# Performance work log

Hardware: AMD Instinct MI355X
Metric: run time of the kernel (lower is better)

Reference implementation:

```python
import jax, jax.numpy as jnp
import numpy as np

D_MODEL, N_HEADS, D_HEAD, D_FF, N_LAYERS, VOCAB = 768, 12, 64, 3072, 4, 32000
B, S = 4, 1024
EPS = 1e-5
NEG = -1000000000.0


def layer_norm(x, gamma, beta):
    mean = jnp.mean(x, axis=-1, keepdims=True)
    var = jnp.mean((x - mean) ** 2, axis=-1, keepdims=True)
    return gamma * ((x - mean) / jnp.sqrt(var + EPS)) + beta


def gelu_lean(x):
    return x * (0.5 * (1.0 + jnp.tanh(0.7978845608 * (x + 0.044715 * x * x * x))))


def positional_encoding(seq_len, dim, dtype):
    idx = jnp.arange(dim)
    exponent = (2 * (idx // 2)).astype(dtype) / float(dim)
    pos = jnp.arange(seq_len, dtype=dtype)[:, None]
    angle = pos / jnp.power(jnp.asarray(10000.0, dtype), exponent[None, :])
    return jnp.where((idx % 2 == 0)[None, :], jnp.sin(angle), jnp.cos(angle))


def setup_inputs() -> dict:
    key = jax.random.key(0)
    ks = jax.random.split(key, 10)
    std = 0.02
    inp = {
        "tokens": jax.random.randint(ks[0], (B, S), 0, VOCAB),
        "predict_idx": 1023,
        "embedding": std * jax.random.normal(ks[1], (D_MODEL, VOCAB), jnp.float32),
        "ln1_g": jnp.ones((N_LAYERS, D_MODEL), jnp.float32),
        "ln1_b": jnp.zeros((N_LAYERS, D_MODEL), jnp.float32),
        "wq": std * jax.random.normal(ks[2], (N_LAYERS, N_HEADS, D_HEAD, D_MODEL), jnp.float32),
        "wk": std * jax.random.normal(ks[3], (N_LAYERS, N_HEADS, D_HEAD, D_MODEL), jnp.float32),
        "wv": std * jax.random.normal(ks[4], (N_LAYERS, N_HEADS, D_HEAD, D_MODEL), jnp.float32),
        "wo": std * jax.random.normal(ks[5], (N_LAYERS, D_MODEL, N_HEADS * D_HEAD), jnp.float32),
        "ln2_g": jnp.ones((N_LAYERS, D_MODEL), jnp.float32),
        "ln2_b": jnp.zeros((N_LAYERS, D_MODEL), jnp.float32),
        "fc1": std * jax.random.normal(ks[6], (N_LAYERS, D_FF, D_MODEL), jnp.float32),
        "fc2": std * jax.random.normal(ks[7], (N_LAYERS, D_MODEL, D_FF), jnp.float32),
        "lnf_g": jnp.ones((D_MODEL,), jnp.float32),
        "lnf_b": jnp.zeros((D_MODEL,), jnp.float32),
        "unembed": std * jax.random.normal(ks[8], (VOCAB, D_MODEL), jnp.float32),
    }
    return inp


def reference(tokens, predict_idx, embedding, ln1_g, ln1_b, wq, wk, wv, wo,
              ln2_g, ln2_b, fc1, fc2, lnf_g, lnf_b, unembed):
    dtype = embedding.dtype
    b, s = tokens.shape
    d_head = wq.shape[2]
    scale = 1.0 / float(np.sqrt(d_head))

    # token embedding [B,S,D] + sinusoidal positions
    x = embedding.T[tokens] + positional_encoding(s, embedding.shape[0], dtype)[None]

    # causal mask: True above the diagonal -> filled with -1e9
    causal = jnp.triu(jnp.ones((s, s), bool), k=1)

    for l in range(wq.shape[0]):
        h = layer_norm(x, ln1_g[l], ln1_b[l])
        q = jnp.einsum('bsd,hed->bhse', h, wq[l])
        k = jnp.einsum('bsd,hed->bhse', h, wk[l])
        v = jnp.einsum('bsd,hed->bhse', h, wv[l])
        scores = jnp.einsum('bhse,bhte->bhst', q, k) * scale
        scores = jnp.where(causal[None, None], NEG, scores)
        weights = jax.nn.softmax(scores, axis=-1)
        attn = jnp.einsum('bhst,bhte->bhse', weights, v)  # [B,H,S,dh]
        attn = attn.transpose(0, 2, 1, 3).reshape(b, s, -1)  # concat heads
        x = x + attn @ wo[l].T
        h2 = layer_norm(x, ln2_g[l], ln2_b[l])
        x = x + gelu_lean(h2 @ fc1[l].T) @ fc2[l].T

    selected = x[:, predict_idx, :]  # [B, D]
    normed = layer_norm(selected, lnf_g, lnf_b)
    return normed @ unembed.T  # [B, vocab]
```

## Files before the change

### kernel.cpp

```cpp
#include <hip/hip_runtime.h>
#include <hip/hip_bf16.h>

#define D_MODEL 768
#define N_HEADS 12
#define D_HEAD  64
#define D_FF    3072
#define N_LAYERS 4
#define VOCAB   32000
#define BATCH   4
#define SEQ     1024
#define NROWS   (BATCH*SEQ)
#define NEGV    -1000000000.0f
#define LN_EPS  1e-5f

typedef __attribute__((ext_vector_type(8))) short bf16x8;
typedef __attribute__((ext_vector_type(4))) float f32x4;
typedef __attribute__((ext_vector_type(8))) unsigned short u16x8;
typedef __attribute__((ext_vector_type(4))) unsigned short u16x4;

typedef __attribute__((address_space(1))) const unsigned int g_u32;
typedef __attribute__((address_space(3))) unsigned int l_u32;

__device__ __forceinline__ float bf2f(unsigned short u) {
  return __uint_as_float(((unsigned int)u) << 16);
}
__device__ __forceinline__ unsigned short f2bf(float f) {
  __hip_bfloat16 h = __float2bfloat16(f);
  return *reinterpret_cast<unsigned short*>(&h);
}

__device__ __forceinline__ float block_reduce_sum(float v, float* sbuf) {
#pragma unroll
  for (int off = 32; off > 0; off >>= 1) v += __shfl_down(v, off, 64);
  int lane = threadIdx.x & 63, wid = threadIdx.x >> 6;
  if (lane == 0) sbuf[wid] = v;
  __syncthreads();
  if (threadIdx.x == 0) sbuf[4] = sbuf[0] + sbuf[1] + sbuf[2] + sbuf[3];
  __syncthreads();
  return sbuf[4];
}

__device__ __forceinline__ float gelu_f(float x) {
  float c = x + 0.044715f * x * x * x;
  return x * (0.5f * (1.0f + tanhf(0.7978845608f * c)));
}

__global__ __launch_bounds__(256) void convert_kernel(
    const float* __restrict__ src, __hip_bfloat16* __restrict__ dst, int n)
{
  int i = (blockIdx.x * 256 + threadIdx.x) * 8;
  if (i >= n) return;
  float4 a = *(const float4*)(src + i);
  float4 b = *(const float4*)(src + i + 4);
  struct bf8 { __hip_bfloat16 h[8]; } r;
  r.h[0] = __float2bfloat16(a.x); r.h[1] = __float2bfloat16(a.y);
  r.h[2] = __float2bfloat16(a.z); r.h[3] = __float2bfloat16(a.w);
  r.h[4] = __float2bfloat16(b.x); r.h[5] = __float2bfloat16(b.y);
  r.h[6] = __float2bfloat16(b.z); r.h[7] = __float2bfloat16(b.w);
  *(bf8*)(dst + i) = r;
}

__global__ __launch_bounds__(256) void qkv_pack_kernel(
    const float* __restrict__ wq, const float* __restrict__ wk,
    const float* __restrict__ wv, __hip_bfloat16* __restrict__ dst)
{
  const int WMAT = D_MODEL * D_MODEL;
  long long i = (long long)(blockIdx.x * 256 + threadIdx.x) * 8;
  long long l = i / (3LL * WMAT);
  long long rem = i - l * 3LL * WMAT;
  int which = (int)(rem / WMAT);
  long long off = rem - (long long)which * WMAT;
  const float* src = (which == 0 ? wq : which == 1 ? wk : wv) + l * WMAT + off;
  float4 a = *(const float4*)src;
  float4 b = *(const float4*)(src + 4);
  struct bf8 { __hip_bfloat16 h[8]; } r;
  r.h[0] = __float2bfloat16(a.x); r.h[1] = __float2bfloat16(a.y);
  r.h[2] = __float2bfloat16(a.z); r.h[3] = __float2bfloat16(a.w);
  r.h[4] = __float2bfloat16(b.x); r.h[5] = __float2bfloat16(b.y);
  r.h[6] = __float2bfloat16(b.z); r.h[7] = __float2bfloat16(b.w);
  *(bf8*)(dst + i) = r;
}

__global__ __launch_bounds__(256) void transpose_emb_kernel(
    const float* __restrict__ emb, __hip_bfloat16* __restrict__ embT)
{
  __shared__ float tile[64][65];
  const int vb = blockIdx.x * 64;
  const int db = blockIdx.y * 64;
  const int tid = threadIdx.x;
  {
    int r = tid >> 4, c = (tid & 15) * 4;
#pragma unroll
    for (int p = 0; p < 4; ++p) {
      float4 v = *(const float4*)(emb + (size_t)(db + r + p * 16) * VOCAB + vb + c);
      tile[c + 0][r + p * 16] = v.x;
      tile[c + 1][r + p * 16] = v.y;
      tile[c + 2][r + p * 16] = v.z;
      tile[c + 3][r + p * 16] = v.w;
    }
  }
  __syncthreads();
  {
    int v = tid >> 2, d0 = (tid & 3) * 16;
    unsigned short* op = (unsigned short*)embT + (size_t)(vb + v) * D_MODEL + db + d0;
    u16x8 o0, o1;
#pragma unroll
    for (int j = 0; j < 8; ++j) {
      o0[j] = f2bf(tile[v][d0 + j]);
      o1[j] = f2bf(tile[v][d0 + 8 + j]);
    }
    *(u16x8*)op = o0;
    *(u16x8*)(op + 8) = o1;
  }
}

__global__ __launch_bounds__(256) void embed_kernel(
    const int* __restrict__ tokens, const __hip_bfloat16* __restrict__ embT,
    float* __restrict__ x)
{
  int bs = blockIdx.x;
  int s = bs & (SEQ - 1);
  int tok = tokens[bs];
  const unsigned short* ep = (const unsigned short*)embT + (size_t)tok * D_MODEL;
  for (int d = threadIdx.x; d < D_MODEL; d += 256) {
    float ev = bf2f(ep[d]);
    int dpair = d & ~1;
    float expo = (float)dpair * (1.0f / (float)D_MODEL);
    float ang = (float)s / powf(10000.0f, expo);
    float pe = (d & 1) ? cosf(ang) : sinf(ang);
    x[(size_t)bs * D_MODEL + d] = ev + pe;
  }
}

__global__ __launch_bounds__(256) void ln_kernel(
    const float* __restrict__ in, __hip_bfloat16* __restrict__ out,
    const float* __restrict__ g, const float* __restrict__ bb)
{
  __shared__ float sbuf[8];
  size_t row = blockIdx.x;
  const float* rp = in + row * D_MODEL;
  int t = threadIdx.x;
  float x0 = rp[t], x1 = rp[t + 256], x2 = rp[t + 512];
  float mean = block_reduce_sum(x0 + x1 + x2, sbuf) * (1.0f / (float)D_MODEL);
  float d0 = x0 - mean, d1 = x1 - mean, d2 = x2 - mean;
  float var = block_reduce_sum(d0*d0 + d1*d1 + d2*d2, sbuf) * (1.0f / (float)D_MODEL);
  float rstd = rsqrtf(var + LN_EPS);
  __hip_bfloat16* op = out + row * D_MODEL;
  op[t]       = __float2bfloat16(g[t]       * (d0 * rstd) + bb[t]);
  op[t + 256] = __float2bfloat16(g[t + 256] * (d1 * rstd) + bb[t + 256]);
  op[t + 512] = __float2bfloat16(g[t + 512] * (d2 * rstd) + bb[t + 512]);
}

__global__ __launch_bounds__(256) void final_ln_kernel(
    const float* __restrict__ x, const int* __restrict__ pidx,
    const float* __restrict__ g, const float* __restrict__ bb,
    float* __restrict__ out)
{
  __shared__ float sbuf[8];
  int p = pidx[0];
  const float* rp = x + ((size_t)blockIdx.x * SEQ + p) * D_MODEL;
  int t = threadIdx.x;
  float x0 = rp[t], x1 = rp[t + 256], x2 = rp[t + 512];
  float mean = block_reduce_sum(x0 + x1 + x2, sbuf) * (1.0f / (float)D_MODEL);
  float d0 = x0 - mean, d1 = x1 - mean, d2 = x2 - mean;
  float var = block_reduce_sum(d0*d0 + d1*d1 + d2*d2, sbuf) * (1.0f / (float)D_MODEL);
  float rstd = rsqrtf(var + LN_EPS);
  float* op = out + (size_t)blockIdx.x * D_MODEL;
  op[t]       = g[t]       * (d0 * rstd) + bb[t];
  op[t + 256] = g[t + 256] * (d1 * rstd) + bb[t + 256];
  op[t + 512] = g[t + 512] * (d2 * rstd) + bb[t + 512];
}

__device__ __forceinline__ int2 xcd_tile(int gx, int gy) {
  int flat = blockIdx.y * gx + blockIdx.x;
  int cpx = (gx * gy) >> 3;
  int logical = (flat & 7) * cpx + (flat >> 3);
  return make_int2(logical % gx, logical / gx);
}

#define WAITV4() asm volatile("s_waitcnt vmcnt(4)" ::: "memory")
#define WAITV2() asm volatile("s_waitcnt vmcnt(2)" ::: "memory")
#define WAITV0() asm volatile("s_waitcnt vmcnt(0)" ::: "memory")
#define MEMFENCE() asm volatile("" ::: "memory")

__global__ __launch_bounds__(256) void gemm_bf16_kernel(
    const __hip_bfloat16* __restrict__ A, const __hip_bfloat16* __restrict__ W,
    void* __restrict__ Cv, const float* __restrict__ resid,
    int N, int K, int mode)
{
  __shared__ __align__(16) unsigned short As[3][128 * 32];
  __shared__ __align__(16) unsigned short Bs[3][128 * 32];
  const unsigned short* Au = (const unsigned short*)A;
  const unsigned short* Wu = (const unsigned short*)W;
  const int tid = threadIdx.x;
  const int wv = tid >> 6, ln = tid & 63;
  const int l15 = ln & 15, l4 = ln >> 4;
  int2 tc = xcd_tile(N >> 7, gridDim.y);
  const int bm = tc.y * 128, bn = tc.x * 128;
  const int wr = wv >> 1, wc = wv & 1;

  const int lrow = wv * 16 + (ln >> 2);
  const int schunk = (ln & 3) ^ ((ln >> 3) & 3);
  const size_t gA0 = (size_t)(bm + lrow) * K + schunk * 8;
  const size_t gA1 = (size_t)(bm + 64 + lrow) * K + schunk * 8;
  const size_t gB0 = (size_t)(bn + lrow) * K + schunk * 8;
  const size_t gB1 = (size_t)(bn + 64 + lrow) * K + schunk * 8;
  const int ldsb = wv * 512;

#define STAGE128(buf, k0)                                                          \
  {                                                                                \
    __builtin_amdgcn_global_load_lds((g_u32*)(Au + gA0 + (k0)), (l_u32*)(As[buf] + ldsb), 16, 0, 0);        \
    __builtin_amdgcn_global_load_lds((g_u32*)(Au + gA1 + (k0)), (l_u32*)(As[buf] + 2048 + ldsb), 16, 0, 0); \
    __builtin_amdgcn_global_load_lds((g_u32*)(Wu + gB0 + (k0)), (l_u32*)(Bs[buf] + ldsb), 16, 0, 0);        \
    __builtin_amdgcn_global_load_lds((g_u32*)(Wu + gB1 + (k0)), (l_u32*)(Bs[buf] + 2048 + ldsb), 16, 0, 0); \
  }

  const int rslot = (l4 ^ ((l15 >> 1) & 3)) * 8;

#define COMPUTE128(buf)                                                            \
  {                                                                                \
    bf16x8 af[4], bfr[4];                                                          \
    _Pragma("unroll")                                                              \
    for (int m = 0; m < 4; ++m)                                                    \
      af[m] = *(const bf16x8*)(As[buf] + (wr * 64 + m * 16 + l15) * 32 + rslot);   \
    _Pragma("unroll")                                                              \
    for (int n = 0; n < 4; ++n)                                                    \
      bfr[n] = *(const bf16x8*)(Bs[buf] + (wc * 64 + n * 16 + l15) * 32 + rslot);  \
    __builtin_amdgcn_s_setprio(1);                                                 \
    _Pragma("unroll")                                                              \
    for (int m = 0; m < 4; ++m)                                                    \
      _Pragma("unroll")                                                            \
      for (int n = 0; n < 4; ++n)                                                  \
        acc[m][n] = __builtin_amdgcn_mfma_f32_16x16x32_bf16(af[m], bfr[n], acc[m][n], 0, 0, 0); \
    __builtin_amdgcn_s_setprio(0);                                                 \
  }

  f32x4 acc[4][4];
#pragma unroll
  for (int m = 0; m < 4; ++m)
#pragma unroll
    for (int n = 0; n < 4; ++n) acc[m][n] = (f32x4){0.f, 0.f, 0.f, 0.f};

  const int NT = K >> 5;
  STAGE128(0, 0);
  STAGE128(1, 32);
  int cur = 0;
  for (int t = 0; t < NT - 1; ++t) {
    WAITV4();
    __builtin_amdgcn_s_barrier();
    MEMFENCE();
    if (t + 2 < NT) {
      int nxt = cur + 2; if (nxt >= 3) nxt -= 3;
      STAGE128(nxt, (t + 2) << 5);
    }
    COMPUTE128(cur);
    cur = (cur == 2) ? 0 : cur + 1;
  }
  WAITV0();
  __builtin_amdgcn_s_barrier();
  MEMFENCE();
  COMPUTE128(cur);

  float* Cf = (float*)Cv;
  __hip_bfloat16* Cb = (__hip_bfloat16*)Cv;
#pragma unroll
  for (int m = 0; m < 4; ++m) {
#pragma unroll
    for (int n = 0; n < 4; ++n) {
#pragma unroll
      for (int r = 0; r < 4; ++r) {
        int row = bm + wr * 64 + m * 16 + l4 * 4 + r;
        int col = bn + wc * 64 + n * 16 + l15;
        size_t off = (size_t)row * N + col;
        float v = acc[m][n][r];
        if (mode == 0)      Cf[off] = v;
        else if (mode == 1) Cf[off] = v + resid[off];
        else if (mode == 2) Cb[off] = __float2bfloat16(v);
        else                Cb[off] = __float2bfloat16(gelu_f(v));
      }
    }
  }
#undef STAGE128
#undef COMPUTE128
}

__global__ __launch_bounds__(256) void gemm64_bf16_kernel(
    const __hip_bfloat16* __restrict__ A, const __hip_bfloat16* __restrict__ W,
    void* __restrict__ Cv, const float* __restrict__ resid,
    int N, int K, int mode)
{
  __shared__ __align__(16) unsigned short As[3][64 * 32];
  __shared__ __align__(16) unsigned short Bs[3][64 * 32];
  const unsigned short* Au = (const unsigned short*)A;
  const unsigned short* Wu = (const unsigned short*)W;
  const int tid = threadIdx.x;
  const int wv = tid >> 6, ln = tid & 63;
  const int l15 = ln & 15, l4 = ln >> 4;
  int2 tc = xcd_tile(N >> 6, gridDim.y);
  const int bm = tc.y * 64, bn = tc.x * 64;
  const int wr = wv >> 1, wc = wv & 1;

  const int lrow = wv * 16 + (ln >> 2);
  const int schunk = (ln & 3) ^ ((ln >> 3) & 3);
  const size_t gA0 = (size_t)(bm + lrow) * K + schunk * 8;
  const size_t gB0 = (size_t)(bn + lrow) * K + schunk * 8;
  const int ldsb = wv * 512;

#define STAGE64(buf, k0)                                                           \
  {                                                                                \
    __builtin_amdgcn_global_load_lds((g_u32*)(Au + gA0 + (k0)), (l_u32*)(As[buf] + ldsb), 16, 0, 0); \
    __builtin_amdgcn_global_load_lds((g_u32*)(Wu + gB0 + (k0)), (l_u32*)(Bs[buf] + ldsb), 16, 0, 0); \
  }

  const int rslot = (l4 ^ ((l15 >> 1) & 3)) * 8;

#define COMPUTE64(buf)                                                             \
  {                                                                                \
    bf16x8 af[2], bfr[2];                                                          \
    _Pragma("unroll")                                                              \
    for (int m = 0; m < 2; ++m)                                                    \
      af[m] = *(const bf16x8*)(As[buf] + (wr * 32 + m * 16 + l15) * 32 + rslot);   \
    _Pragma("unroll")                                                              \
    for (int n = 0; n < 2; ++n)                                                    \
      bfr[n] = *(const bf16x8*)(Bs[buf] + (wc * 32 + n * 16 + l15) * 32 + rslot);  \
    __builtin_amdgcn_s_setprio(1);                                                 \
    _Pragma("unroll")                                                              \
    for (int m = 0; m < 2; ++m)                                                    \
      _Pragma("unroll")                                                            \
      for (int n = 0; n < 2; ++n)                                                  \
        acc[m][n] = __builtin_amdgcn_mfma_f32_16x16x32_bf16(af[m], bfr[n], acc[m][n], 0, 0, 0); \
    __builtin_amdgcn_s_setprio(0);                                                 \
  }

  f32x4 acc[2][2];
#pragma unroll
  for (int m = 0; m < 2; ++m)
#pragma unroll
    for (int n = 0; n < 2; ++n) acc[m][n] = (f32x4){0.f, 0.f, 0.f, 0.f};

  const int NT = K >> 5;
  STAGE64(0, 0);
  STAGE64(1, 32);
  int cur = 0;
  for (int t = 0; t < NT - 1; ++t) {
    WAITV2();
    __builtin_amdgcn_s_barrier();
    MEMFENCE();
    if (t + 2 < NT) {
      int nxt = cur + 2; if (nxt >= 3) nxt -= 3;
      STAGE64(nxt, (t + 2) << 5);
    }
    COMPUTE64(cur);
    cur = (cur == 2) ? 0 : cur + 1;
  }
  WAITV0();
  __builtin_amdgcn_s_barrier();
  MEMFENCE();
  COMPUTE64(cur);

  float* Cf = (float*)Cv;
  __hip_bfloat16* Cb = (__hip_bfloat16*)Cv;
#pragma unroll
  for (int m = 0; m < 2; ++m) {
#pragma unroll
    for (int n = 0; n < 2; ++n) {
#pragma unroll
      for (int r = 0; r < 4; ++r) {
        int row = bm + wr * 32 + m * 16 + l4 * 4 + r;
        int col = bn + wc * 32 + n * 16 + l15;
        size_t off = (size_t)row * N + col;
        float v = acc[m][n][r];
        if (mode == 0)      Cf[off] = v;
        else if (mode == 1) Cf[off] = v + resid[off];
        else if (mode == 2) Cb[off] = __float2bfloat16(v);
        else                Cb[off] = __float2bfloat16(gelu_f(v));
      }
    }
  }
#undef STAGE64
#undef COMPUTE64
}

__global__ __launch_bounds__(128) void flash_attn_kernel(
    const __hip_bfloat16* __restrict__ qkv_, __hip_bfloat16* __restrict__ attn_)
{
  const unsigned short* qkv = (const unsigned short*)qkv_;
  unsigned short* attn = (unsigned short*)attn_;
  const int px = blockIdx.x;
  const int h  = blockIdx.y;
  const int b  = blockIdx.z;
  const int tid = threadIdx.x;
  const int wq = tid >> 6, ln = tid & 63;
  const int l15 = ln & 15, l4 = ln >> 4;

  __shared__ unsigned short Ks[2][64 * 64];
  __shared__ unsigned short Vt[2][64 * 64];
  __shared__ unsigned short Pw[2][16 * 64];

  const int krow = tid >> 3;
  const int kchunk = (tid & 7) ^ ((tid >> 3) & 7);
  const int kldsbase = (tid & 64) * 8;

  const int vc = tid & 7;
  const int vp = tid >> 3;
  const int vtr = (2 * vp) & 7;
  const int vtb0 = vp >> 2;

  u16x8 v0, v1, v2, v3;

#define STAGE_K(buf, t0)                                                           \
  {                                                                                \
    _Pragma("unroll")                                                              \
    for (int j = 0; j < 4; ++j) {                                                  \
      const unsigned short* gk = qkv +                                             \
          (size_t)(b * SEQ + (t0) + j * 16 + krow) * 2304 + 768 + h * 64 + kchunk * 8; \
      __builtin_amdgcn_global_load_lds((g_u32*)gk,                                 \
          (l_u32*)(Ks[buf] + j * 1024 + kldsbase), 16, 0, 0);                      \
    }                                                                              \
  }

#define LOAD_V(t0)                                                                 \
  {                                                                                \
    const unsigned short* gv = qkv +                                               \
        (size_t)(b * SEQ + (t0) + 2 * vp) * 2304 + 1536 + h * 64 + vc * 8;         \
    v0 = *(const u16x8*)gv;                                                        \
    v1 = *(const u16x8*)(gv + 2304);                                               \
    v2 = *(const u16x8*)(gv + 32 * 2304);                                          \
    v3 = *(const u16x8*)(gv + 33 * 2304);                                          \
  }

#define WRITE_VT(buf)                                                              \
  {                                                                                \
    _Pragma("unroll")                                                              \
    for (int j = 0; j < 8; ++j) {                                                  \
      int e = vc * 8 + j;                                                          \
      unsigned int w01 = (unsigned int)(unsigned short)v0[j] |                     \
                         ((unsigned int)(unsigned short)v1[j] << 16);              \
      unsigned int w23 = (unsigned int)(unsigned short)v2[j] |                     \
                         ((unsigned int)(unsigned short)v3[j] << 16);              \
      *(unsigned int*)(Vt[buf] + e * 64 + ((vtb0 ^ (e & 7)) << 3) + vtr) = w01;    \
      *(unsigned int*)(Vt[buf] + e * 64 + (((vtb0 + 4) ^ (e & 7)) << 3) + vtr) = w23; \
    }                                                                              \
  }

  for (int pass = 0; pass < 2; ++pass) {
    const int qi = (pass == 0) ? px : 31 - px;
    const int s0 = qi * 32;
    const int ntiles = (qi >> 1) + 1;
    const int qg = s0 + wq * 16 + l15;

    bf16x8 qf[2];
    {
      const size_t qbase = (size_t)(b * SEQ + qg) * 2304 + h * 64;
#pragma unroll
      for (int ks = 0; ks < 2; ++ks) {
        u16x8 raw = *(const u16x8*)(qkv + qbase + ks * 32 + l4 * 8);
        bf16x8 q;
#pragma unroll
        for (int j = 0; j < 8; ++j) q[j] = (short)f2bf(bf2f(raw[j]) * 0.125f);
        qf[ks] = q;
      }
    }

    float mrow = -1e30f, lrow = 0.f;
    f32x4 o[4];
#pragma unroll
    for (int n = 0; n < 4; ++n) o[n] = (f32x4){0.f, 0.f, 0.f, 0.f};

    STAGE_K(0, 0);
    LOAD_V(0);
    WAITV0();
    WRITE_VT(0);
    __syncthreads();

    for (int t = 0; t < ntiles; ++t) {
      const int cur = t & 1;
      const bool pfn = (t + 1 < ntiles);
      if (pfn) { STAGE_K(cur ^ 1, (t + 1) * 64); LOAD_V((t + 1) * 64); }

      f32x4 sf[4];
#pragma unroll
      for (int n = 0; n < 4; ++n) sf[n] = (f32x4){0.f, 0.f, 0.f, 0.f};
#pragma unroll
      for (int ks = 0; ks < 2; ++ks) {
#pragma unroll
        for (int n = 0; n < 4; ++n) {
          int tr = n * 16 + l15;
          bf16x8 kf = *(const bf16x8*)(Ks[cur] + tr * 64 + (((ks * 4 + l4) ^ (tr & 7)) << 3));
          sf[n] = __builtin_amdgcn_mfma_f32_16x16x32_bf16(kf, qf[ks], sf[n], 0, 0, 0);
        }
      }

      if (t == ntiles - 1) {
#pragma unroll
        for (int n = 0; n < 4; ++n) {
#pragma unroll
          for (int r = 0; r < 4; ++r) {
            int tg = t * 64 + n * 16 + l4 * 4 + r;
            if (tg > qg) sf[n][r] = NEGV;
          }
        }
      }

      float mx = sf[0][0];
#pragma unroll
      for (int n = 0; n < 4; ++n)
#pragma unroll
        for (int r = 0; r < 4; ++r) mx = fmaxf(mx, sf[n][r]);
      mx = fmaxf(mx, __shfl_xor(mx, 16));
      mx = fmaxf(mx, __shfl_xor(mx, 32));
      float mnew = fmaxf(mrow, mx);
      float alpha = __expf(mrow - mnew);
      float pb[4][4];
      float sum = 0.f;
#pragma unroll
      for (int n = 0; n < 4; ++n)
#pragma unroll
        for (int r = 0; r < 4; ++r) {
          float p = __expf(sf[n][r] - mnew);
          pb[n][r] = p;
          sum += p;
        }
      sum += __shfl_xor(sum, 16);
      sum += __shfl_xor(sum, 32);
      lrow = lrow * alpha + sum;
      mrow = mnew;

      float ar[4];
#pragma unroll
      for (int r = 0; r < 4; ++r)
        ar[r] = __shfl(alpha, (ln & 48) | (l4 * 4 + r));
#pragma unroll
      for (int n = 0; n < 4; ++n)
#pragma unroll
        for (int r = 0; r < 4; ++r) o[n][r] *= ar[r];

      unsigned short* Pme = Pw[wq];
#pragma unroll
      for (int n = 0; n < 4; ++n) {
        int tb = 2 * n + (l4 >> 1);
        u16x4 w;
        w[0] = f2bf(pb[n][0]); w[1] = f2bf(pb[n][1]);
        w[2] = f2bf(pb[n][2]); w[3] = f2bf(pb[n][3]);
        *(u16x4*)(Pme + l15 * 64 + ((tb ^ (l15 & 7)) << 3) + (l4 & 1) * 4) = w;
      }

#pragma unroll
      for (int ks = 0; ks < 2; ++ks) {
        bf16x8 pf = *(const bf16x8*)(Pme + l15 * 64 + (((ks * 4 + l4) ^ (l15 & 7)) << 3));
#pragma unroll
        for (int n = 0; n < 4; ++n) {
          int e = n * 16 + l15;
          bf16x8 vf = *(const bf16x8*)(Vt[cur] + e * 64 + (((ks * 4 + l4) ^ (e & 7)) << 3));
          o[n] = __builtin_amdgcn_mfma_f32_16x16x32_bf16(pf, vf, o[n], 0, 0, 0);
        }
      }

      if (pfn) { WAITV0(); WRITE_VT(cur ^ 1); }
      __syncthreads();
    }

    float lr[4];
#pragma unroll
    for (int r = 0; r < 4; ++r)
      lr[r] = __shfl(lrow, (ln & 48) | (l4 * 4 + r));
#pragma unroll
    for (int r = 0; r < 4; ++r) {
      float inv = 1.0f / lr[r];
      size_t base = (size_t)(b * SEQ + s0 + wq * 16 + l4 * 4 + r) * D_MODEL + h * 64;
#pragma unroll
      for (int n = 0; n < 4; ++n)
        attn[base + n * 16 + l15] = f2bf(o[n][r] * inv);
    }
  }
#undef STAGE_K
#undef LOAD_V
#undef WRITE_VT
}

__global__ __launch_bounds__(256) void logits_kernel(
    const float* __restrict__ normed, const float* __restrict__ unemb,
    float* __restrict__ out)
{
  __shared__ __align__(16) float ns[BATCH][D_MODEL];
  for (int d = threadIdx.x; d < BATCH * D_MODEL; d += 256)
    ((float*)ns)[d] = normed[d];
  __syncthreads();
  int g = threadIdx.x >> 4, li = threadIdx.x & 15;
  int v = blockIdx.x * 16 + g;
  const float* up = unemb + (size_t)v * D_MODEL;
  float s0 = 0.f, s1 = 0.f, s2 = 0.f, s3 = 0.f;
#pragma unroll
  for (int it = 0; it < D_MODEL / 64; ++it) {
    int e = it * 64 + li * 4;
    float4 u = *(const float4*)(up + e);
    float4 n0 = *(const float4*)&ns[0][e];
    float4 n1 = *(const float4*)&ns[1][e];
    float4 n2 = *(const float4*)&ns[2][e];
    float4 n3 = *(const float4*)&ns[3][e];
    s0 += u.x*n0.x + u.y*n0.y + u.z*n0.z + u.w*n0.w;
    s1 += u.x*n1.x + u.y*n1.y + u.z*n1.z + u.w*n1.w;
    s2 += u.x*n2.x + u.y*n2.y + u.z*n2.z + u.w*n2.w;
    s3 += u.x*n3.x + u.y*n3.y + u.z*n3.z + u.w*n3.w;
  }
#pragma unroll
  for (int msk = 1; msk < 16; msk <<= 1) {
    s0 += __shfl_xor(s0, msk, 64); s1 += __shfl_xor(s1, msk, 64);
    s2 += __shfl_xor(s2, msk, 64); s3 += __shfl_xor(s3, msk, 64);
  }
  if (li == 0) {
    out[(size_t)0 * VOCAB + v] = s0;
    out[(size_t)1 * VOCAB + v] = s1;
    out[(size_t)2 * VOCAB + v] = s2;
    out[(size_t)3 * VOCAB + v] = s3;
  }
}

extern "C" void kernel_launch(void* const* d_in, const int* in_sizes, int n_in,
                              void* d_out, int out_size, void* d_ws, size_t ws_size,
                              hipStream_t stream) {
  const int*   tokens = (const int*)d_in[0];
  const int*   pidx   = (const int*)d_in[1];
  const float* emb    = (const float*)d_in[2];
  const float* ln1_g  = (const float*)d_in[3];
  const float* ln1_b  = (const float*)d_in[4];
  const float* wq     = (const float*)d_in[5];
  const float* wk     = (const float*)d_in[6];
  const float* wv     = (const float*)d_in[7];
  const float* wo     = (const float*)d_in[8];
  const float* ln2_g  = (const float*)d_in[9];
  const float* ln2_b  = (const float*)d_in[10];
  const float* fc1    = (const float*)d_in[11];
  const float* fc2    = (const float*)d_in[12];
  const float* lnf_g  = (const float*)d_in[13];
  const float* lnf_b  = (const float*)d_in[14];
  const float* unemb  = (const float*)d_in[15];
  float* out = (float*)d_out;

  char* wp = (char*)d_ws;
  const size_t NX = (size_t)NROWS * D_MODEL;
  float* x = (float*)wp;                  wp += NX * 4;
  float* normed = (float*)wp;             wp += BATCH * D_MODEL * 4;
  __hip_bfloat16* h    = (__hip_bfloat16*)wp; wp += NX * 2;
  __hip_bfloat16* attn = (__hip_bfloat16*)wp; wp += NX * 2;
  __hip_bfloat16* qkvb = (__hip_bfloat16*)wp; wp += (size_t)NROWS * 2304 * 2;
  __hip_bfloat16* ffn  = (__hip_bfloat16*)wp; wp += (size_t)NROWS * D_FF * 2;
  __hip_bfloat16* wqkvb = (__hip_bfloat16*)wp; wp += (size_t)N_LAYERS * 2304 * D_MODEL * 2;
  __hip_bfloat16* wob   = (__hip_bfloat16*)wp; wp += (size_t)N_LAYERS * D_MODEL * D_MODEL * 2;
  __hip_bfloat16* fc1b  = (__hip_bfloat16*)wp; wp += (size_t)N_LAYERS * D_FF * D_MODEL * 2;
  __hip_bfloat16* fc2b  = (__hip_bfloat16*)wp; wp += (size_t)N_LAYERS * D_MODEL * D_FF * 2;

  __hip_bfloat16* embT = attn;

  const int WMAT = D_MODEL * D_MODEL;
  const int FMAT = D_FF * D_MODEL;

  transpose_emb_kernel<<<dim3(VOCAB / 64, D_MODEL / 64), 256, 0, stream>>>(emb, embT);
  embed_kernel<<<NROWS, 256, 0, stream>>>(tokens, embT, x);

  qkv_pack_kernel<<<N_LAYERS * 3 * WMAT / 2048, 256, 0, stream>>>(wq, wk, wv, wqkvb);
  convert_kernel<<<N_LAYERS * WMAT / 2048, 256, 0, stream>>>(wo,  wob,  N_LAYERS * WMAT);
  convert_kernel<<<N_LAYERS * FMAT / 2048, 256, 0, stream>>>(fc1, fc1b, N_LAYERS * FMAT);
  convert_kernel<<<N_LAYERS * FMAT / 2048, 256, 0, stream>>>(fc2, fc2b, N_LAYERS * FMAT);

  for (int l = 0; l < N_LAYERS; ++l) {
    const size_t qofs = (size_t)l * 3 * WMAT;
    const size_t wofs = (size_t)l * WMAT;
    const size_t fofs = (size_t)l * FMAT;

    ln_kernel<<<NROWS, 256, 0, stream>>>(x, h, ln1_g + l * D_MODEL, ln1_b + l * D_MODEL);

    gemm_bf16_kernel<<<dim3(2304 / 128, NROWS / 128), 256, 0, stream>>>(
        h, wqkvb + qofs, qkvb, nullptr, 2304, D_MODEL, 2);

    flash_attn_kernel<<<dim3(16, N_HEADS, BATCH), 128, 0, stream>>>(qkvb, attn);

    gemm64_bf16_kernel<<<dim3(D_MODEL / 64, NROWS / 64), 256, 0, stream>>>(
        attn, wob + wofs, x, x, D_MODEL, D_MODEL, 1);

    ln_kernel<<<NROWS, 256, 0, stream>>>(x, h, ln2_g + l * D_MODEL, ln2_b + l * D_MODEL);

    gemm_bf16_kernel<<<dim3(D_FF / 128, NROWS / 128), 256, 0, stream>>>(
        h, fc1b + fofs, ffn, nullptr, D_FF, D_MODEL, 3);

    gemm64_bf16_kernel<<<dim3(D_MODEL / 64, NROWS / 64), 256, 0, stream>>>(
        ffn, fc2b + fofs, x, x, D_MODEL, D_FF, 1);
  }

  final_ln_kernel<<<BATCH, 256, 0, stream>>>(x, pidx, lnf_g, lnf_b, normed);
  logits_kernel<<<VOCAB / 16, 256, 0, stream>>>(normed, unemb, out);
}
```

Before: 871.5 us.

## Use 128-tile GEMM for projections, fuse weight converts, cheaper GELU

Replaces the 64x64-tile GEMM with the 128x128-tile kernel for the attention output and FFN down projections, which cuts the number of blocks from 768 to 192 and increases data reuse per block. The three weight conversion launches are merged into a single kernel that relies on wob, fc1b and fc2b sitting contiguously in the workspace. GELU is rewritten as x*sigmoid(2z) using __expf in place of tanhf. The risk is that 192 blocks may underfill the GPU's compute units.

```diff
diff --git a/kernel.cpp b/kernel.cpp
--- a/kernel.cpp
+++ b/kernel.cpp
@@ -41,23 +41,8 @@
 }
 
 __device__ __forceinline__ float gelu_f(float x) {
-  float c = x + 0.044715f * x * x * x;
-  return x * (0.5f * (1.0f + tanhf(0.7978845608f * c)));
-}
-
-__global__ __launch_bounds__(256) void convert_kernel(
-    const float* __restrict__ src, __hip_bfloat16* __restrict__ dst, int n)
-{
-  int i = (blockIdx.x * 256 + threadIdx.x) * 8;
-  if (i >= n) return;
-  float4 a = *(const float4*)(src + i);
-  float4 b = *(const float4*)(src + i + 4);
-  struct bf8 { __hip_bfloat16 h[8]; } r;
-  r.h[0] = __float2bfloat16(a.x); r.h[1] = __float2bfloat16(a.y);
-  r.h[2] = __float2bfloat16(a.z); r.h[3] = __float2bfloat16(a.w);
-  r.h[4] = __float2bfloat16(b.x); r.h[5] = __float2bfloat16(b.y);
-  r.h[6] = __float2bfloat16(b.z); r.h[7] = __float2bfloat16(b.w);
-  *(bf8*)(dst + i) = r;
+  float z2 = 1.5957691216f * x * (1.0f + 0.044715f * x * x);
+  return x / (1.0f + __expf(-z2));
 }
 
 __global__ __launch_bounds__(256) void qkv_pack_kernel(
@@ -81,6 +66,27 @@
   *(bf8*)(dst + i) = r;
 }
 
+__global__ __launch_bounds__(256) void convert3_kernel(
+    const float* __restrict__ wo, const float* __restrict__ fc1,
+    const float* __restrict__ fc2, __hip_bfloat16* __restrict__ dst)
+{
+  const long long WM4 = 4LL * D_MODEL * D_MODEL;
+  const long long FM4 = 4LL * D_FF * D_MODEL;
+  long long i = (long long)(blockIdx.x * 256 + threadIdx.x) * 8;
+  const float* src;
+  if (i < WM4)            src = wo  + i;
+  else if (i < WM4 + FM4) src = fc1 + (i - WM4);
+  else                    src = fc2 + (i - WM4 - FM4);
+  float4 a = *(const float4*)src;
+  float4 b = *(const float4*)(src + 4);
+  struct bf8 { __hip_bfloat16 h[8]; } r;
+  r.h[0] = __float2bfloat16(a.x); r.h[1] = __float2bfloat16(a.y);
+  r.h[2] = __float2bfloat16(a.z); r.h[3] = __float2bfloat16(a.w);
+  r.h[4] = __float2bfloat16(b.x); r.h[5] = __float2bfloat16(b.y);
+  r.h[6] = __float2bfloat16(b.z); r.h[7] = __float2bfloat16(b.w);
+  *(bf8*)(dst + i) = r;
+}
+
 __global__ __launch_bounds__(256) void transpose_emb_kernel(
     const float* __restrict__ emb, __hip_bfloat16* __restrict__ embT)
 {
@@ -179,7 +185,6 @@
 }
 
 #define WAITV4() asm volatile("s_waitcnt vmcnt(4)" ::: "memory")
-#define WAITV2() asm volatile("s_waitcnt vmcnt(2)" ::: "memory")
 #define WAITV0() asm volatile("s_waitcnt vmcnt(0)" ::: "memory")
 #define MEMFENCE() asm volatile("" ::: "memory")
 
@@ -282,103 +287,6 @@
   }
 #undef STAGE128
 #undef COMPUTE128
-}
-
-__global__ __launch_bounds__(256) void gemm64_bf16_kernel(
-    const __hip_bfloat16* __restrict__ A, const __hip_bfloat16* __restrict__ W,
-    void* __restrict__ Cv, const float* __restrict__ resid,
-    int N, int K, int mode)
-{
-  __shared__ __align__(16) unsigned short As[3][64 * 32];
-  __shared__ __align__(16) unsigned short Bs[3][64 * 32];
-  const unsigned short* Au = (const unsigned short*)A;
-  const unsigned short* Wu = (const unsigned short*)W;
-  const int tid = threadIdx.x;
-  const int wv = tid >> 6, ln = tid & 63;
-  const int l15 = ln & 15, l4 = ln >> 4;
-  int2 tc = xcd_tile(N >> 6, gridDim.y);
-  const int bm = tc.y * 64, bn = tc.x * 64;
-  const int wr = wv >> 1, wc = wv & 1;
-
-  const int lrow = wv * 16 + (ln >> 2);
-  const int schunk = (ln & 3) ^ ((ln >> 3) & 3);
-  const size_t gA0 = (size_t)(bm + lrow) * K + schunk * 8;
-  const size_t gB0 = (size_t)(bn + lrow) * K + schunk * 8;
-  const int ldsb = wv * 512;
-
-#define STAGE64(buf, k0)                                                           \
-  {                                                                                \
-    __builtin_amdgcn_global_load_lds((g_u32*)(Au + gA0 + (k0)), (l_u32*)(As[buf] + ldsb), 16, 0, 0); \
-    __builtin_amdgcn_global_load_lds((g_u32*)(Wu + gB0 + (k0)), (l_u32*)(Bs[buf] + ldsb), 16, 0, 0); \
-  }
-
-  const int rslot = (l4 ^ ((l15 >> 1) & 3)) * 8;
-
-#define COMPUTE64(buf)                                                             \
-  {                                                                                \
-    bf16x8 af[2], bfr[2];                                                          \
-    _Pragma("unroll")                                                              \
-    for (int m = 0; m < 2; ++m)                                                    \
-      af[m] = *(const bf16x8*)(As[buf] + (wr * 32 + m * 16 + l15) * 32 + rslot);   \
-    _Pragma("unroll")                                                              \
-    for (int n = 0; n < 2; ++n)                                                    \
-      bfr[n] = *(const bf16x8*)(Bs[buf] + (wc * 32 + n * 16 + l15) * 32 + rslot);  \
-    __builtin_amdgcn_s_setprio(1);                                                 \
-    _Pragma("unroll")                                                              \
-    for (int m = 0; m < 2; ++m)                                                    \
-      _Pragma("unroll")                                                            \
-      for (int n = 0; n < 2; ++n)                                                  \
-        acc[m][n] = __builtin_amdgcn_mfma_f32_16x16x32_bf16(af[m], bfr[n], acc[m][n], 0, 0, 0); \
-    __builtin_amdgcn_s_setprio(0);                                                 \
-  }
-
-  f32x4 acc[2][2];
-#pragma unroll
-  for (int m = 0; m < 2; ++m)
-#pragma unroll
-    for (int n = 0; n < 2; ++n) acc[m][n] = (f32x4){0.f, 0.f, 0.f, 0.f};
-
-  const int NT = K >> 5;
-  STAGE64(0, 0);
-  STAGE64(1, 32);
-  int cur = 0;
-  for (int t = 0; t < NT - 1; ++t) {
-    WAITV2();
-    __builtin_amdgcn_s_barrier();
-    MEMFENCE();
-    if (t + 2 < NT) {
-      int nxt = cur + 2; if (nxt >= 3) nxt -= 3;
-      STAGE64(nxt, (t + 2) << 5);
-    }
-    COMPUTE64(cur);
-    cur = (cur == 2) ? 0 : cur + 1;
-  }
-  WAITV0();
-  __builtin_amdgcn_s_barrier();
-  MEMFENCE();
-  COMPUTE64(cur);
-
-  float* Cf = (float*)Cv;
-  __hip_bfloat16* Cb = (__hip_bfloat16*)Cv;
-#pragma unroll
-  for (int m = 0; m < 2; ++m) {
-#pragma unroll
-    for (int n = 0; n < 2; ++n) {
-#pragma unroll
-      for (int r = 0; r < 4; ++r) {
-        int row = bm + wr * 32 + m * 16 + l4 * 4 + r;
-        int col = bn + wc * 32 + n * 16 + l15;
-        size_t off = (size_t)row * N + col;
-        float v = acc[m][n][r];
-        if (mode == 0)      Cf[off] = v;
-        else if (mode == 1) Cf[off] = v + resid[off];
-        else if (mode == 2) Cb[off] = __float2bfloat16(v);
-        else                Cb[off] = __float2bfloat16(gelu_f(v));
-      }
-    }
-  }
-#undef STAGE64
-#undef COMPUTE64
 }
 
 __global__ __launch_bounds__(128) void flash_attn_kernel(
@@ -659,9 +567,7 @@
   embed_kernel<<<NROWS, 256, 0, stream>>>(tokens, embT, x);
 
   qkv_pack_kernel<<<N_LAYERS * 3 * WMAT / 2048, 256, 0, stream>>>(wq, wk, wv, wqkvb);
-  convert_kernel<<<N_LAYERS * WMAT / 2048, 256, 0, stream>>>(wo,  wob,  N_LAYERS * WMAT);
-  convert_kernel<<<N_LAYERS * FMAT / 2048, 256, 0, stream>>>(fc1, fc1b, N_LAYERS * FMAT);
-  convert_kernel<<<N_LAYERS * FMAT / 2048, 256, 0, stream>>>(fc2, fc2b, N_LAYERS * FMAT);
+  convert3_kernel<<<(N_LAYERS * (WMAT + 2 * FMAT)) / 2048, 256, 0, stream>>>(wo, fc1, fc2, wob);
 
   for (int l = 0; l < N_LAYERS; ++l) {
     const size_t qofs = (size_t)l * 3 * WMAT;
@@ -675,7 +581,7 @@
 
     flash_attn_kernel<<<dim3(16, N_HEADS, BATCH), 128, 0, stream>>>(qkvb, attn);
 
-    gemm64_bf16_kernel<<<dim3(D_MODEL / 64, NROWS / 64), 256, 0, stream>>>(
+    gemm_bf16_kernel<<<dim3(D_MODEL / 128, NROWS / 128), 256, 0, stream>>>(
         attn, wob + wofs, x, x, D_MODEL, D_MODEL, 1);
 
     ln_kernel<<<NROWS, 256, 0, stream>>>(x, h, ln2_g + l * D_MODEL, ln2_b + l * D_MODEL);
@@ -683,7 +589,7 @@
     gemm_bf16_kernel<<<dim3(D_FF / 128, NROWS / 128), 256, 0, stream>>>(
         h, fc1b + fofs, ffn, nullptr, D_FF, D_MODEL, 3);
 
-    gemm64_bf16_kernel<<<dim3(D_MODEL / 64, NROWS / 64), 256, 0, stream>>>(
+    gemm_bf16_kernel<<<dim3(D_MODEL / 128, NROWS / 128), 256, 0, stream>>>(
         ffn, fc2b + fofs, x, x, D_MODEL, D_FF, 1);
   }
 
```

Result: slower. 1.005 ms (+15.3%).
